# Performance work log

Hardware: AMD Instinct MI355X
Metric: run time of the kernel (lower is better)

Reference implementation:

```python
import jax, jax.numpy as jnp
import numpy as np

D, H, E = 1024, 4096, 8


def setup_inputs() -> dict:
    key = jax.random.key(0)
    ks = jax.random.split(key, 8)
    s_in = 1.0 / np.sqrt(D)
    s_hid = 1.0 / np.sqrt(H)
    return {
        "x": jax.random.normal(ks[0], (4, 2048, D), dtype=jnp.float32),
        # torch nn.Linear init ~ U(-1/sqrt(fan_in), 1/sqrt(fan_in)); exact dist irrelevant for a numeric reference
        "Wg": jax.random.uniform(ks[1], (D, E), jnp.float32, -s_in, s_in),
        "bg": jax.random.uniform(ks[2], (E,), jnp.float32, -s_in, s_in),
        "W1": jax.random.uniform(ks[3], (E, D, H), jnp.float32, -s_in, s_in),
        "b1": jax.random.uniform(ks[4], (E, H), jnp.float32, -s_in, s_in),
        "W2": jax.random.uniform(ks[5], (E, H, D), jnp.float32, -s_hid, s_hid),
        "b2": jax.random.uniform(ks[6], (E, D), jnp.float32, -s_hid, s_hid),
    }


def reference(x, Wg, bg, W1, b1, W2, b2):
    # gate
    gate_logits = jnp.einsum("bsd,de->bse", x, Wg) + bg
    gate_probs = jax.nn.softmax(gate_logits, axis=-1)
    expert_indices = jnp.argmax(gate_probs, axis=-1)  # [B,S]

    # Faithful to source: mask the INPUT per expert, run the full MLP on the
    # masked input (biases still apply to zeroed tokens!), and sum all experts.
    onehot = jax.nn.one_hot(expert_indices, E, dtype=x.dtype)  # [B,S,E]
    xm = jnp.einsum("bsd,bse->ebsd", x, onehot)                # [E,B,S,D]
    h = jax.nn.relu(jnp.einsum("ebsd,edh->ebsh", xm, W1) + b1[:, None, None, :])
    out_e = jnp.einsum("ebsh,ehd->ebsd", h, W2) + b2[:, None, None, :]
    combined_output = jnp.sum(out_e, axis=0)                   # [B,S,D]
    return combined_output, gate_probs, expert_indices
```

## Files before the change

kernel.cpp:

```cpp
#include <hip/hip_runtime.h>
#include <hip/hip_bf16.h>
#include <cstdint>

#define D_DIM 1024
#define H_DIM 4096
#define E_NUM 8
#define NTOK  8192

#define BM 128
#define BN 128
#define BK 32

#define MAXT 72
#define NBY1 (H_DIM / BN)
#define NBY2 (D_DIM / BN)

typedef __bf16 bf16;
typedef __bf16 bf16x8 __attribute__((ext_vector_type(8)));
typedef __bf16 bf16x4 __attribute__((ext_vector_type(4)));
typedef float  f32x4  __attribute__((ext_vector_type(4)));

#define GLOAD16(g, l)                                                          \
    __builtin_amdgcn_global_load_lds(                                          \
        (const __attribute__((address_space(1))) void*)(g),                    \
        (__attribute__((address_space(3))) void*)(l), 16, 0, 0)


__global__ __launch_bounds__(256) void zero_kernel(int* cnt, float* cpartial)
{
    const int i = blockIdx.x * 256 + threadIdx.x;
    if (i < E_NUM * D_DIM) cpartial[i] = 0.f;
    if (i < E_NUM) cnt[i] = 0;
}

__global__ __launch_bounds__(256) void fused_aux_kernel(
    const float* __restrict__ W2, const float* __restrict__ W1,
    const float* __restrict__ b1,
    const float* __restrict__ x, const float* __restrict__ Wg,
    const float* __restrict__ bg,
    bf16* __restrict__ W2t, bf16* __restrict__ W1t,
    float* __restrict__ cpartial,
    float* __restrict__ out_probs, float* __restrict__ out_idx,
    int* __restrict__ cnt, int* __restrict__ list)
{
    __shared__ float T[64][65];
    const int b = blockIdx.x;
    const int t = threadIdx.x;

    if (b < 8192) {
        const int kx = b & 63, ny = (b >> 6) & 15, e = b >> 10;
        const int k0 = kx * 64, n0 = ny * 64;
        const float* src = W2 + (size_t)e * H_DIM * D_DIM;
        {
            const int ty = t >> 4, tx = (t & 15) * 4;
#pragma unroll
            for (int i = 0; i < 4; i++) {
                f32x4 v = __builtin_nontemporal_load(
                    (const f32x4*)(src + (size_t)(k0 + ty + 16 * i) * D_DIM + n0 + tx));
                T[ty + 16 * i][tx + 0] = v[0]; T[ty + 16 * i][tx + 1] = v[1];
                T[ty + 16 * i][tx + 2] = v[2]; T[ty + 16 * i][tx + 3] = v[3];
            }
        }
        __syncthreads();
        {
            bf16* dtile = W2t + (size_t)e * H_DIM * D_DIM
                        + ((size_t)ny * (H_DIM / 64) + kx) * 4096;
            const int n = t >> 2, kk = (t & 3) * 16;
            bf16 tmp[16];
#pragma unroll
            for (int j = 0; j < 16; j++) tmp[j] = (bf16)T[kk + j][n];
            *(bf16x8*)(dtile + n * 64 + kk)     = *(bf16x8*)&tmp[0];
            *(bf16x8*)(dtile + n * 64 + kk + 8) = *(bf16x8*)&tmp[8];
        }
        if (t < 64) {
            float s = 0.f;
#pragma unroll 8
            for (int h = 0; h < 64; h++)
                s += fmaxf(b1[(size_t)e * H_DIM + k0 + h], 0.f) * T[h][t];
            atomicAdd(&cpartial[(size_t)e * D_DIM + n0 + t], s);
        }
    } else if (b < 16384) {
        const int i2 = b - 8192;
        const int kx = i2 & 15, ny = (i2 >> 4) & 63, e = i2 >> 10;
        const int k0 = kx * 64, n0 = ny * 64;
        const float* src = W1 + (size_t)e * D_DIM * H_DIM;
        {
            const int ty = t >> 4, tx = (t & 15) * 4;
#pragma unroll
            for (int i = 0; i < 4; i++) {
                f32x4 v = __builtin_nontemporal_load(
                    (const f32x4*)(src + (size_t)(k0 + ty + 16 * i) * H_DIM + n0 + tx));
                T[ty + 16 * i][tx + 0] = v[0]; T[ty + 16 * i][tx + 1] = v[1];
                T[ty + 16 * i][tx + 2] = v[2]; T[ty + 16 * i][tx + 3] = v[3];
            }
        }
        __syncthreads();
        {
            bf16* dtile = W1t + (size_t)e * D_DIM * H_DIM
                        + ((size_t)ny * (D_DIM / 64) + kx) * 4096;
            const int n = t >> 2, kk = (t & 3) * 16;
            bf16 tmp[16];
#pragma unroll
            for (int j = 0; j < 16; j++) tmp[j] = (bf16)T[kk + j][n];
            *(bf16x8*)(dtile + n * 64 + kk)     = *(bf16x8*)&tmp[0];
            *(bf16x8*)(dtile + n * 64 + kk + 8) = *(bf16x8*)&tmp[8];
        }
    } else {
        const int tok = (b - 16384) * 4 + (t >> 6);
        const int l = t & 63;
        double part[E_NUM];
#pragma unroll
        for (int e = 0; e < E_NUM; e++) part[e] = 0.0;
        const float* xr = x + (size_t)tok * D_DIM;
#pragma unroll
        for (int i = 0; i < D_DIM / 64; i++) {
            const int d = l + i * 64;
            const float xv = xr[d];
            const float* wr = Wg + (size_t)d * E_NUM;
            float4 w0 = *(const float4*)(wr);
            float4 w1 = *(const float4*)(wr + 4);
            part[0] += (double)xv * (double)w0.x;
            part[1] += (double)xv * (double)w0.y;
            part[2] += (double)xv * (double)w0.z;
            part[3] += (double)xv * (double)w0.w;
            part[4] += (double)xv * (double)w1.x;
            part[5] += (double)xv * (double)w1.y;
            part[6] += (double)xv * (double)w1.z;
            part[7] += (double)xv * (double)w1.w;
        }
#pragma unroll
        for (int e = 0; e < E_NUM; e++) {
            double v = part[e];
            for (int s = 32; s > 0; s >>= 1) v += __shfl_xor(v, s, 64);
            part[e] = v;
        }
        if (l == 0) {
            float logits[E_NUM], probs[E_NUM];
            float m = -3.0e38f;
#pragma unroll
            for (int e = 0; e < E_NUM; e++) {
                logits[e] = (float)(part[e] + (double)bg[e]);
                m = fmaxf(m, logits[e]);
            }
            float s = 0.f;
#pragma unroll
            for (int e = 0; e < E_NUM; e++) { probs[e] = expf(logits[e] - m); s += probs[e]; }
            const float inv = 1.f / s;
            int best = 0; float bp = -1.f;
#pragma unroll
            for (int e = 0; e < E_NUM; e++) {
                probs[e] *= inv;
                if (probs[e] > bp) { bp = probs[e]; best = e; }
            }
#pragma unroll
            for (int e = 0; e < E_NUM; e++) out_probs[(size_t)tok * E_NUM + e] = probs[e];
            out_idx[tok] = (float)best;
            const int pos = atomicAdd(&cnt[best], 1);
            list[best * NTOK + pos] = tok;
        }
    }
}

__global__ void offsets_kernel(const int* __restrict__ cnt, int* __restrict__ off,
                               int* __restrict__ tile_e, int* __restrict__ tile_row,
                               int* __restrict__ tile_n)
{
    if (threadIdx.x == 0) {
        int a = 0, n = 0;
        for (int e = 0; e < E_NUM; e++) {
            off[e] = a; a += cnt[e];
            for (int rr = 0; rr < cnt[e]; rr += BM) {
                tile_e[n] = e; tile_row[n] = rr; n++;
            }
        }
        tile_n[0] = n;
    }
}

__global__ __launch_bounds__(256) void gather_kernel(
    const float* __restrict__ x, const int* __restrict__ off,
    const int* __restrict__ cnt, const int* __restrict__ list,
    bf16* __restrict__ Xg,
    const float* __restrict__ cpartial, const float* __restrict__ b2,
    float* __restrict__ adj)
{
    const int p = blockIdx.x;
    const int t = threadIdx.x;
    if (p >= NTOK) {
        const int d = (p - NTOK) * 256 + t;
        float c[E_NUM];
        float tot = 0.f;
#pragma unroll
        for (int e = 0; e < E_NUM; e++) {
            c[e] = cpartial[(size_t)e * D_DIM + d] + b2[(size_t)e * D_DIM + d];
            tot += c[e];
        }
#pragma unroll
        for (int e = 0; e < E_NUM; e++) adj[(size_t)e * D_DIM + d] = tot - c[e];
        return;
    }
    int e = 0;
    while (e < E_NUM - 1 && p >= off[e] + cnt[e]) e++;
    const int token = list[e * NTOK + (p - off[e])];
    const float* src = x + (size_t)token * D_DIM;
    bf16* dst = Xg + (size_t)p * D_DIM;
    float4 v = *(const float4*)(src + t * 4);
    bf16x4 o;
    o[0] = (bf16)v.x; o[1] = (bf16)v.y; o[2] = (bf16)v.z; o[3] = (bf16)v.w;
    *(bf16x4*)(dst + t * 4) = o;
}

__global__ __launch_bounds__(256) void gemm1_kernel(
    const bf16* __restrict__ Xg, const bf16* __restrict__ W1t,
    const float* __restrict__ b1, const int* __restrict__ cnt,
    const int* __restrict__ off, const int* __restrict__ tile_e,
    const int* __restrict__ tile_row, const int* __restrict__ tile_n,
    bf16* __restrict__ Hb)
{
    const int orig = blockIdx.x;
    const int q = (MAXT * NBY1) >> 3;
    const int fid = (orig & 7) * q + (orig >> 3);
    const int tx = fid % MAXT;
    const int by = fid / MAXT;
    if (tx >= tile_n[0]) return;
    const int e  = tile_e[tx];
    const int m0 = tile_row[tx];
    const int ne = cnt[e];
    const int oe = off[e];

    __shared__ bf16 As[BM * BK];
    __shared__ bf16 Bs[BN * BK];

    const int t = threadIdx.x;
    const int w = t >> 6, lane = t & 63;
    const int wr = w >> 1, wc = w & 1;
    const int lrow = lane & 15, kq = (lane >> 4) * 8;

    const int lr = lane >> 2;
    const int lc = (lane & 3) * 8;
    const bf16* Ast = Xg + ((size_t)(oe + m0 + w * 32 + lr)) * D_DIM + lc;
    bf16* Alds = As + (w * 32) * BK;
    bf16* Blds = Bs + (w * 32) * BK;

    const int r0 = w * 32 + lr, r1 = r0 + 16;
    const bf16* Bb0 = W1t + (size_t)e * D_DIM * H_DIM
                    + ((size_t)(by * 2 + (r0 >> 6)) * (D_DIM / 64)) * 4096
                    + (r0 & 63) * 64 + lc;
    const bf16* Bb1 = W1t + (size_t)e * D_DIM * H_DIM
                    + ((size_t)(by * 2 + (r1 >> 6)) * (D_DIM / 64)) * 4096
                    + (r1 & 63) * 64 + lc;

    f32x4 acc[4][4];
#pragma unroll
    for (int m = 0; m < 4; m++)
#pragma unroll
        for (int n = 0; n < 4; n++) acc[m][n] = (f32x4){0.f, 0.f, 0.f, 0.f};

    for (int kt = 0; kt < D_DIM / BK; kt++) {
        const int kc = kt * BK;
        const int boff = (kt >> 1) * 4096 + (kt & 1) * 32;
        GLOAD16(Ast + kc,              Alds);
        GLOAD16(Ast + 16 * D_DIM + kc, Alds + 16 * BK);
        GLOAD16(Bb0 + boff,            Blds);
        GLOAD16(Bb1 + boff,            Blds + 16 * BK);
        __syncthreads();

        bf16x8 af[4], bfr[4];
#pragma unroll
        for (int m = 0; m < 4; m++)
            af[m] = *(const bf16x8*)&As[(wr * 64 + m * 16 + lrow) * BK + kq];
#pragma unroll
        for (int n = 0; n < 4; n++)
            bfr[n] = *(const bf16x8*)&Bs[(wc * 64 + n * 16 + lrow) * BK + kq];
#pragma unroll
        for (int m = 0; m < 4; m++)
#pragma unroll
            for (int n = 0; n < 4; n++)
                acc[m][n] = __builtin_amdgcn_mfma_f32_16x16x32_bf16(af[m], bfr[n], acc[m][n], 0, 0, 0);
        __syncthreads();
    }

#pragma unroll
    for (int m = 0; m < 4; m++) {
        const int rb0 = m0 + wr * 64 + m * 16 + ((lane >> 4) << 2);
#pragma unroll
        for (int n = 0; n < 4; n++) {
            const int gcol = by * BN + wc * 64 + n * 16 + (lane & 15);
            const float bias = b1[(size_t)e * H_DIM + gcol];
#pragma unroll
            for (int r = 0; r < 4; r++) {
                const int grow = rb0 + r;
                if (grow < ne) {
                    float v = acc[m][n][r] + bias;
                    Hb[((size_t)(oe + grow)) * H_DIM + gcol] = (bf16)fmaxf(v, 0.f);
                }
            }
        }
    }
}

__global__ __launch_bounds__(256) void gemm2_kernel(
    const bf16* __restrict__ Hb, const bf16* __restrict__ W2t,
    const float* __restrict__ b2, const float* __restrict__ adj,
    const int* __restrict__ cnt, const int* __restrict__ off,
    const int* __restrict__ tile_e, const int* __restrict__ tile_row,
    const int* __restrict__ tile_n, const int* __restrict__ list,
    float* __restrict__ out)
{
    const int orig = blockIdx.x;
    const int q = (MAXT * NBY2) >> 3;
    const int fid = (orig & 7) * q + (orig >> 3);
    const int tx = fid % MAXT;
    const int by = fid / MAXT;
    if (tx >= tile_n[0]) return;
    const int e  = tile_e[tx];
    const int m0 = tile_row[tx];
    const int ne = cnt[e];
    const int oe = off[e];

    __shared__ bf16 As[BM * BK];
    __shared__ bf16 Bs[BN * BK];

    const int t = threadIdx.x;
    const int w = t >> 6, lane = t & 63;
    const int wr = w >> 1, wc = w & 1;
    const int lrow = lane & 15, kq = (lane >> 4) * 8;

    const int lr = lane >> 2;
    const int lc = (lane & 3) * 8;
    const bf16* Ast = Hb + ((size_t)(oe + m0 + w * 32 + lr)) * H_DIM + lc;
    bf16* Alds = As + (w * 32) * BK;
    bf16* Blds = Bs + (w * 32) * BK;

    const int r0 = w * 32 + lr, r1 = r0 + 16;
    const bf16* Bb0 = W2t + (size_t)e * D_DIM * H_DIM
                    + ((size_t)(by * 2 + (r0 >> 6)) * (H_DIM / 64)) * 4096
                    + (r0 & 63) * 64 + lc;
    const bf16* Bb1 = W2t + (size_t)e * D_DIM * H_DIM
                    + ((size_t)(by * 2 + (r1 >> 6)) * (H_DIM / 64)) * 4096
                    + (r1 & 63) * 64 + lc;

    f32x4 acc[4][4];
#pragma unroll
    for (int m = 0; m < 4; m++)
#pragma unroll
        for (int n = 0; n < 4; n++) acc[m][n] = (f32x4){0.f, 0.f, 0.f, 0.f};

    for (int kt = 0; kt < H_DIM / BK; kt++) {
        const int kc = kt * BK;
        const int boff = (kt >> 1) * 4096 + (kt & 1) * 32;
        GLOAD16(Ast + kc,              Alds);
        GLOAD16(Ast + 16 * H_DIM + kc, Alds + 16 * BK);
        GLOAD16(Bb0 + boff,            Blds);
        GLOAD16(Bb1 + boff,            Blds + 16 * BK);
        __syncthreads();

        bf16x8 af[4], bfr[4];
#pragma unroll
        for (int m = 0; m < 4; m++)
            af[m] = *(const bf16x8*)&As[(wr * 64 + m * 16 + lrow) * BK + kq];
#pragma unroll
        for (int n = 0; n < 4; n++)
            bfr[n] = *(const bf16x8*)&Bs[(wc * 64 + n * 16 + lrow) * BK + kq];
#pragma unroll
        for (int m = 0; m < 4; m++)
#pragma unroll
            for (int n = 0; n < 4; n++)
                acc[m][n] = __builtin_amdgcn_mfma_f32_16x16x32_bf16(af[m], bfr[n], acc[m][n], 0, 0, 0);
        __syncthreads();
    }

#pragma unroll
    for (int m = 0; m < 4; m++) {
        const int rb0 = m0 + wr * 64 + m * 16 + ((lane >> 4) << 2);
#pragma unroll
        for (int n = 0; n < 4; n++) {
            const int gcol = by * BN + wc * 64 + n * 16 + (lane & 15);
            const float badj = b2[(size_t)e * D_DIM + gcol] + adj[(size_t)e * D_DIM + gcol];
#pragma unroll
            for (int r = 0; r < 4; r++) {
                const int grow = rb0 + r;
                if (grow < ne) {
                    const int tok = list[e * NTOK + grow];
                    out[(size_t)tok * D_DIM + gcol] = acc[m][n][r] + badj;
                }
            }
        }
    }
}

extern "C" void kernel_launch(void* const* d_in, const int* in_sizes, int n_in,
                              void* d_out, int out_size, void* d_ws, size_t ws_size,
                              hipStream_t stream)
{
    (void)in_sizes; (void)n_in; (void)out_size; (void)ws_size;
    const float* x  = (const float*)d_in[0];
    const float* Wg = (const float*)d_in[1];
    const float* bg = (const float*)d_in[2];
    const float* W1 = (const float*)d_in[3];
    const float* b1 = (const float*)d_in[4];
    const float* W2 = (const float*)d_in[5];
    const float* b2 = (const float*)d_in[6];

    float* out_comb  = (float*)d_out;
    float* out_probs = out_comb + (size_t)NTOK * D_DIM;
    float* out_idx   = out_probs + (size_t)NTOK * E_NUM;

    char* ws = (char*)d_ws;
    size_t o = 0;
    bf16* W1t = (bf16*)(ws + o); o += (size_t)E_NUM * H_DIM * D_DIM * 2;
    bf16* W2t = (bf16*)(ws + o); o += (size_t)E_NUM * H_DIM * D_DIM * 2;
    bf16* Hb  = (bf16*)(ws + o); o += (size_t)NTOK * H_DIM * 2;
    bf16* Xg  = (bf16*)(ws + o); o += (size_t)NTOK * D_DIM * 2;
    float* cpartial = (float*)(ws + o); o += (size_t)E_NUM * D_DIM * 4;
    float* adj      = (float*)(ws + o); o += (size_t)E_NUM * D_DIM * 4;
    int* cnt  = (int*)(ws + o); o += 256;
    int* off  = (int*)(ws + o); o += 256;
    int* tile_e   = (int*)(ws + o); o += 512;
    int* tile_row = (int*)(ws + o); o += 512;
    int* tile_n   = (int*)(ws + o); o += 256;
    int* list = (int*)(ws + o); o += (size_t)E_NUM * NTOK * 4;

    zero_kernel<<<(E_NUM * D_DIM + 255) / 256, 256, 0, stream>>>(cnt, cpartial);
    fused_aux_kernel<<<18432, 256, 0, stream>>>(W2, W1, b1, x, Wg, bg,
                                                W2t, W1t, cpartial,
                                                out_probs, out_idx, cnt, list);
    offsets_kernel<<<1, 64, 0, stream>>>(cnt, off, tile_e, tile_row, tile_n);
    gather_kernel<<<NTOK + D_DIM / 256, 256, 0, stream>>>(x, off, cnt, list, Xg,
                                                          cpartial, b2, adj);
    gemm1_kernel<<<MAXT * NBY1, 256, 0, stream>>>(Xg, W1t, b1, cnt, off, tile_e, tile_row, tile_n, Hb);
    gemm2_kernel<<<MAXT * NBY2, 256, 0, stream>>>(Hb, W2t, b2, adj, cnt, off, tile_e, tile_row, tile_n, list, out_comb);
}
```

Baseline: 417.0 us.

## Restructure weight transpose-convert into wide row slabs with bf16 LDS staging

The weight transpose/convert blocks now each read a 16-row slab spanning full 1024-wide rows, so global reads become long contiguous streams. The slab is converted to bf16 before it is written to shared memory, halving LDS traffic, and each block writes many 64x64 tiles. The block count drops from 16384 to 2560 weight blocks. The relu(b1)·W2 partial sum is now computed from bf16-rounded values rather than fp32, which slightly changes the numerics of the bias correction. Writes become 32-byte pieces scattered across tiles, and fewer, larger blocks may reduce parallelism.

Measured after the change: 446.4 us. 7.1% more time.

```diff
diff --git a/kernel.cpp b/kernel.cpp
--- a/kernel.cpp
+++ b/kernel.cpp
@@ -15,6 +15,10 @@
 #define NBY1 (H_DIM / BN)
 #define NBY2 (D_DIM / BN)
 
+#define NW1B 512
+#define NW2B 2048
+#define NAUX (NW1B + NW2B + 2048)
+
 typedef __bf16 bf16;
 typedef __bf16 bf16x8 __attribute__((ext_vector_type(8)));
 typedef __bf16 bf16x4 __attribute__((ext_vector_type(4)));
@@ -24,7 +28,6 @@
     __builtin_amdgcn_global_load_lds(                                          \
         (const __attribute__((address_space(1))) void*)(g),                    \
         (__attribute__((address_space(3))) void*)(l), 16, 0, 0)
-
 
 __global__ __launch_bounds__(256) void zero_kernel(int* cnt, float* cpartial)
 {
@@ -43,70 +46,81 @@
     float* __restrict__ out_probs, float* __restrict__ out_idx,
     int* __restrict__ cnt, int* __restrict__ list)
 {
-    __shared__ float T[64][65];
+    __shared__ bf16 T[16][1032];
     const int b = blockIdx.x;
     const int t = threadIdx.x;
 
-    if (b < 8192) {
-        const int kx = b & 63, ny = (b >> 6) & 15, e = b >> 10;
-        const int k0 = kx * 64, n0 = ny * 64;
-        const float* src = W2 + (size_t)e * H_DIM * D_DIM;
-        {
-            const int ty = t >> 4, tx = (t & 15) * 4;
-#pragma unroll
-            for (int i = 0; i < 4; i++) {
+    if (b < NW1B) {
+        const int e = b >> 6, slab = b & 63;
+        const int d0 = slab * 16;
+        const float* src = W1 + (size_t)e * D_DIM * H_DIM + (size_t)d0 * H_DIM;
+        const int kx = d0 >> 6, kk = d0 & 63;
+        for (int hc = 0; hc < 4; hc++) {
+#pragma unroll
+            for (int c = 0; c < 16; c++) {
+                const int f = c * 256 + t;
+                const int row = f >> 8, col4 = (f & 255) * 4;
                 f32x4 v = __builtin_nontemporal_load(
-                    (const f32x4*)(src + (size_t)(k0 + ty + 16 * i) * D_DIM + n0 + tx));
-                T[ty + 16 * i][tx + 0] = v[0]; T[ty + 16 * i][tx + 1] = v[1];
-                T[ty + 16 * i][tx + 2] = v[2]; T[ty + 16 * i][tx + 3] = v[3];
-            }
+                    (const f32x4*)(src + (size_t)row * H_DIM + hc * 1024 + col4));
+                bf16x4 o; o[0] = (bf16)v[0]; o[1] = (bf16)v[1];
+                o[2] = (bf16)v[2]; o[3] = (bf16)v[3];
+                *(bf16x4*)&T[row][col4] = o;
+            }
+            __syncthreads();
+#pragma unroll
+            for (int w = 0; w < 4; w++) {
+                const int p = w * 256 + t;
+                const int ti = p >> 6, n = p & 63;
+                const int ny = hc * 16 + ti;
+                bf16* dtile = W1t + (size_t)e * D_DIM * H_DIM
+                            + ((size_t)ny * (D_DIM / 64) + kx) * 4096;
+                bf16 tmp[16];
+#pragma unroll
+                for (int j = 0; j < 16; j++) tmp[j] = T[j][ti * 64 + n];
+                *(bf16x8*)(dtile + n * 64 + kk)     = *(bf16x8*)&tmp[0];
+                *(bf16x8*)(dtile + n * 64 + kk + 8) = *(bf16x8*)&tmp[8];
+            }
+            __syncthreads();
+        }
+    } else if (b < NW1B + NW2B) {
+        const int b2 = b - NW1B;
+        const int e = b2 >> 8, slab = b2 & 255;
+        const int k0 = slab * 16;
+        const float* src = W2 + (size_t)e * H_DIM * D_DIM + (size_t)k0 * D_DIM;
+        const int kx = k0 >> 6, kk = k0 & 63;
+        float rb1[16];
+#pragma unroll
+        for (int j = 0; j < 16; j++)
+            rb1[j] = fmaxf(b1[(size_t)e * H_DIM + k0 + j], 0.f);
+#pragma unroll
+        for (int c = 0; c < 16; c++) {
+            const int f = c * 256 + t;
+            const int row = f >> 8, col4 = (f & 255) * 4;
+            f32x4 v = __builtin_nontemporal_load(
+                (const f32x4*)(src + (size_t)row * D_DIM + col4));
+            bf16x4 o; o[0] = (bf16)v[0]; o[1] = (bf16)v[1];
+            o[2] = (bf16)v[2]; o[3] = (bf16)v[3];
+            *(bf16x4*)&T[row][col4] = o;
         }
         __syncthreads();
-        {
+#pragma unroll
+        for (int w = 0; w < 4; w++) {
+            const int p = w * 256 + t;
+            const int ti = p >> 6, n = p & 63;
             bf16* dtile = W2t + (size_t)e * H_DIM * D_DIM
-                        + ((size_t)ny * (H_DIM / 64) + kx) * 4096;
-            const int n = t >> 2, kk = (t & 3) * 16;
+                        + ((size_t)ti * (H_DIM / 64) + kx) * 4096;
             bf16 tmp[16];
 #pragma unroll
-            for (int j = 0; j < 16; j++) tmp[j] = (bf16)T[kk + j][n];
+            for (int j = 0; j < 16; j++) tmp[j] = T[j][ti * 64 + n];
             *(bf16x8*)(dtile + n * 64 + kk)     = *(bf16x8*)&tmp[0];
             *(bf16x8*)(dtile + n * 64 + kk + 8) = *(bf16x8*)&tmp[8];
-        }
-        if (t < 64) {
             float s = 0.f;
-#pragma unroll 8
-            for (int h = 0; h < 64; h++)
-                s += fmaxf(b1[(size_t)e * H_DIM + k0 + h], 0.f) * T[h][t];
-            atomicAdd(&cpartial[(size_t)e * D_DIM + n0 + t], s);
-        }
-    } else if (b < 16384) {
-        const int i2 = b - 8192;
-        const int kx = i2 & 15, ny = (i2 >> 4) & 63, e = i2 >> 10;
-        const int k0 = kx * 64, n0 = ny * 64;
-        const float* src = W1 + (size_t)e * D_DIM * H_DIM;
-        {
-            const int ty = t >> 4, tx = (t & 15) * 4;
-#pragma unroll
-            for (int i = 0; i < 4; i++) {
-                f32x4 v = __builtin_nontemporal_load(
-                    (const f32x4*)(src + (size_t)(k0 + ty + 16 * i) * H_DIM + n0 + tx));
-                T[ty + 16 * i][tx + 0] = v[0]; T[ty + 16 * i][tx + 1] = v[1];
-                T[ty + 16 * i][tx + 2] = v[2]; T[ty + 16 * i][tx + 3] = v[3];
-            }
-        }
-        __syncthreads();
-        {
-            bf16* dtile = W1t + (size_t)e * D_DIM * H_DIM
-                        + ((size_t)ny * (D_DIM / 64) + kx) * 4096;
-            const int n = t >> 2, kk = (t & 3) * 16;
-            bf16 tmp[16];
-#pragma unroll
-            for (int j = 0; j < 16; j++) tmp[j] = (bf16)T[kk + j][n];
-            *(bf16x8*)(dtile + n * 64 + kk)     = *(bf16x8*)&tmp[0];
-            *(bf16x8*)(dtile + n * 64 + kk + 8) = *(bf16x8*)&tmp[8];
+#pragma unroll
+            for (int j = 0; j < 16; j++) s += rb1[j] * (float)tmp[j];
+            atomicAdd(&cpartial[(size_t)e * D_DIM + ti * 64 + n], s);
         }
     } else {
-        const int tok = (b - 16384) * 4 + (t >> 6);
+        const int tok = (b - NW1B - NW2B) * 4 + (t >> 6);
         const int l = t & 63;
         double part[E_NUM];
 #pragma unroll
@@ -422,9 +436,9 @@
     int* list = (int*)(ws + o); o += (size_t)E_NUM * NTOK * 4;
 
     zero_kernel<<<(E_NUM * D_DIM + 255) / 256, 256, 0, stream>>>(cnt, cpartial);
-    fused_aux_kernel<<<18432, 256, 0, stream>>>(W2, W1, b1, x, Wg, bg,
-                                                W2t, W1t, cpartial,
-                                                out_probs, out_idx, cnt, list);
+    fused_aux_kernel<<<NAUX, 256, 0, stream>>>(W2, W1, b1, x, Wg, bg,
+                                               W2t, W1t, cpartial,
+                                               out_probs, out_idx, cnt, list);
     offsets_kernel<<<1, 64, 0, stream>>>(cnt, off, tile_e, tile_row, tile_n);
     gather_kernel<<<NTOK + D_DIM / 256, 256, 0, stream>>>(x, off, cnt, list, Xg,
                                                           cpartial, b2, adj);
```
